# Kernel optimization log

Measured on AMD Instinct MI355X. Metric: run time of the kernel, lower is better.

## Reference

```python
import jax, jax.numpy as jnp
import numpy as np

TIME_STEP = 101  # module stores time_step + 1 with init arg time_step=100


def setup_inputs() -> dict:
    key = jax.random.key(0)
    x = jax.random.normal(key, (8, 4096, 1024), dtype=jnp.float32)
    return {"x": x, "use_gpu": 0}


def reference(x, use_gpu):
    # x: [B, S, D]
    S, D = x.shape[1], x.shape[2]
    dt = x.dtype
    pos = jnp.arange(S, dtype=dt)[:, None]              # [S, 1]
    i = jnp.arange(D, dtype=dt)[None, :]                # [1, D]
    # NOTE: original code uses the raw index i (not i//2) in the exponent.
    div = jnp.power(jnp.asarray(10000.0, dt), 2.0 * i / D)  # [1, D]
    ang_pos = pos / div                                  # [S, D]
    ang_t = jnp.asarray(TIME_STEP, dt) / div             # [1, D]
    even = (jnp.arange(D) % 2 == 0)[None, :]             # [1, D]
    pe = jnp.where(even,
                   jnp.sin(ang_pos) + jnp.sin(ang_t),
                   jnp.cos(ang_pos) + jnp.cos(ang_t))    # [S, D]
    return x + pe[None, :, :]
```

## Files before the change

### kernel.cpp

```cpp
#include <hip/hip_runtime.h>


typedef float f32x4 __attribute__((ext_vector_type(4)));

#define TWO_PI   6.283185307179586f
#define INV_2PI  0.15915494309189535f

__device__ __forceinline__ float fast_sin(float a) {
    float k = rintf(a * INV_2PI);
    float r = fmaf(-k, TWO_PI, a);
    return __sinf(r);
}
__device__ __forceinline__ float fast_cos(float a) {
    float k = rintf(a * INV_2PI);
    float r = fmaf(-k, TWO_PI, a);
    return __cosf(r);
}

__global__ __launch_bounds__(256) void tpe_kernel(const float* __restrict__ x,
                                                  float* __restrict__ out) {
    constexpr int S = 4096;
    constexpr int D = 1024;
    constexpr int B = 8;

    const int s  = blockIdx.x;
    const int d0 = threadIdx.x * 4;

    const size_t base = (size_t)s * D + (size_t)d0;
    constexpr size_t bstride = (size_t)S * (size_t)D;

    f32x4 v[8];
#pragma unroll
    for (int b = 0; b < B; ++b)
        v[b] = *reinterpret_cast<const f32x4*>(x + base + (size_t)b * bstride);

    constexpr float C = 13.287712379549449f * 2.0f / (float)D;
    const float pos = (float)s;
    float pe[4];
#pragma unroll
    for (int j = 0; j < 4; ++j) {
        const int d = d0 + j;
        const float rdiv = exp2f(-C * (float)d);
        const float ap = pos * rdiv;
        const float at = 101.0f * rdiv;
        if ((d & 1) == 0)
            pe[j] = fast_sin(ap) + fast_sin(at);
        else
            pe[j] = fast_cos(ap) + fast_cos(at);
    }

#pragma unroll
    for (int b = 0; b < B; ++b) {
        f32x4 ov;
        ov.x = v[b].x + pe[0];
        ov.y = v[b].y + pe[1];
        ov.z = v[b].z + pe[2];
        ov.w = v[b].w + pe[3];
        __builtin_nontemporal_store(
            ov, reinterpret_cast<f32x4*>(out + base + (size_t)b * bstride));
    }
}

extern "C" void kernel_launch(void* const* d_in, const int* in_sizes, int n_in,
                              void* d_out, int out_size, void* d_ws, size_t ws_size,
                              hipStream_t stream) {
    const float* x = (const float*)d_in[0];
    float* out = (float*)d_out;
    tpe_kernel<<<4096, 256, 0, stream>>>(x, out);
}
```

Baseline: 48.77 us.

## Process consecutive sequence rows per block using angle-addition recurrence for PE

Each block now handles 8 consecutive flattened rows (same batch, adjacent positions) instead of the same position across 8 batches. The positional sin/cos for successive rows comes from the angle-addition identity using sin/cos of rdiv, so transcendental evaluation happens once per block rather than per row. The change also swaps nontemporal stores for regular stores. The recurrence can accumulate rounding error across the 8 steps, and the kernel still launches 4096 blocks, which matches the total row count of 32768/8.

```diff
diff --git a/kernel.cpp b/kernel.cpp
--- a/kernel.cpp
+++ b/kernel.cpp
@@ -8,56 +8,60 @@
 
 __device__ __forceinline__ float fast_sin(float a) {
     float k = rintf(a * INV_2PI);
-    float r = fmaf(-k, TWO_PI, a);
-    return __sinf(r);
+    return __sinf(fmaf(-k, TWO_PI, a));
 }
 __device__ __forceinline__ float fast_cos(float a) {
     float k = rintf(a * INV_2PI);
-    float r = fmaf(-k, TWO_PI, a);
-    return __cosf(r);
+    return __cosf(fmaf(-k, TWO_PI, a));
 }
 
 __global__ __launch_bounds__(256) void tpe_kernel(const float* __restrict__ x,
                                                   float* __restrict__ out) {
-    constexpr int S = 4096;
-    constexpr int D = 1024;
-    constexpr int B = 8;
+    constexpr int D    = 1024;
+    constexpr int ROWS = 8;
 
-    const int s  = blockIdx.x;
-    const int d0 = threadIdx.x * 4;
+    const int tid = threadIdx.x;
+    const long long row0 = (long long)blockIdx.x * ROWS;
+    const int s0 = (int)(row0 & 4095);
+    const int d0 = tid * 4;
 
-    const size_t base = (size_t)s * D + (size_t)d0;
-    constexpr size_t bstride = (size_t)S * (size_t)D;
+    const float* xp = x   + row0 * D + d0;
+    float*       op = out + row0 * D + d0;
 
-    f32x4 v[8];
+    f32x4 v[ROWS];
 #pragma unroll
-    for (int b = 0; b < B; ++b)
-        v[b] = *reinterpret_cast<const f32x4*>(x + base + (size_t)b * bstride);
+    for (int r = 0; r < ROWS; ++r)
+        v[r] = *reinterpret_cast<const f32x4*>(xp + (size_t)r * D);
 
-    constexpr float C = 13.287712379549449f * 2.0f / (float)D;
-    const float pos = (float)s;
-    float pe[4];
+    constexpr float C = 2.0f * 13.287712379549449f / (float)D;
+    float sp[4], cp[4], sr[4], cr[4], tterm[4];
 #pragma unroll
     for (int j = 0; j < 4; ++j) {
-        const int d = d0 + j;
-        const float rdiv = exp2f(-C * (float)d);
-        const float ap = pos * rdiv;
+        const float rdiv = exp2f(-C * (float)(d0 + j));
+        const float ap = (float)s0 * rdiv;
+        sp[j] = fast_sin(ap);
+        cp[j] = fast_cos(ap);
+        sr[j] = __sinf(rdiv);
+        cr[j] = __cosf(rdiv);
         const float at = 101.0f * rdiv;
-        if ((d & 1) == 0)
-            pe[j] = fast_sin(ap) + fast_sin(at);
-        else
-            pe[j] = fast_cos(ap) + fast_cos(at);
+        tterm[j] = ((j & 1) == 0) ? fast_sin(at) : fast_cos(at);
     }
 
 #pragma unroll
-    for (int b = 0; b < B; ++b) {
+    for (int r = 0; r < ROWS; ++r) {
         f32x4 ov;
-        ov.x = v[b].x + pe[0];
-        ov.y = v[b].y + pe[1];
-        ov.z = v[b].z + pe[2];
-        ov.w = v[b].w + pe[3];
-        __builtin_nontemporal_store(
-            ov, reinterpret_cast<f32x4*>(out + base + (size_t)b * bstride));
+        ov.x = v[r].x + sp[0] + tterm[0];
+        ov.y = v[r].y + cp[1] + tterm[1];
+        ov.z = v[r].z + sp[2] + tterm[2];
+        ov.w = v[r].w + cp[3] + tterm[3];
+        *reinterpret_cast<f32x4*>(op + (size_t)r * D) = ov;
+
+#pragma unroll
+        for (int j = 0; j < 4; ++j) {
+            const float ns = fmaf(sp[j], cr[j],  cp[j] * sr[j]);
+            const float nc = fmaf(cp[j], cr[j], -sp[j] * sr[j]);
+            sp[j] = ns; cp[j] = nc;
+        }
     }
 }
 
```

New measurement: 44.15 us. -9.5%, faster.
